# Kernel optimization log

Hardware: AMD Instinct MI355X
Metric: run time of the kernel (lower is better)

The kernel has to match this reference:

```python
import jax, jax.numpy as jnp
import numpy as np

B, T, H, V = 256, 256, 512, 32000
L = 3  # stacked LSTM layers


def setup_inputs() -> dict:
    key = jax.random.key(0)
    ks = jax.random.split(key, 12)
    s = 0.05
    n = lambda k, shp: (jax.random.normal(k, shp, jnp.float32) * s)
    return {
        "text_1": jax.random.randint(ks[0], (B, T), 0, V, dtype=jnp.int32),
        "text_2": jax.random.randint(ks[1], (B, T), 0, V, dtype=jnp.int32),
        "text_3": jax.random.randint(ks[2], (B, T), 0, V, dtype=jnp.int32),
        "emb": n(ks[3], (V, H)),
        "Wx": n(ks[4], (L, H, 4 * H)),
        "Wh": n(ks[5], (L, H, 4 * H)),
        "b": jnp.zeros((L, 4 * H), jnp.float32),
        "g1": jnp.ones((3 * H,), jnp.float32), "beta1": jnp.zeros((3 * H,), jnp.float32),
        "W1": n(ks[6], (3 * H, 2 * H)), "bd1": jnp.zeros((2 * H,), jnp.float32),
        "g2": jnp.ones((2 * H,), jnp.float32), "beta2": jnp.zeros((2 * H,), jnp.float32),
        "W2": n(ks[7], (2 * H, H // 5)), "bd2": jnp.zeros((H // 5,), jnp.float32),
        "g3": jnp.ones((H // 5,), jnp.float32), "beta3": jnp.zeros((H // 5,), jnp.float32),
        "W3": n(ks[8], (H // 5, 4)), "bd3": jnp.zeros((4,), jnp.float32),
    }


def _lstm_stack(tokens, emb, Wx, Wh, b):
    # tokens: [B, T] int -> last hidden of top layer [B, H]
    x = emb[tokens]                      # [B, T, H]
    x = jnp.transpose(x, (1, 0, 2))      # [T, B, H] (scan over time)
    bsz, h = x.shape[1], Wh.shape[1]
    for l in range(Wx.shape[0]):
        Wx_l, Wh_l, b_l = Wx[l], Wh[l], b[l]
        def step(carry, xt):
            hprev, cprev = carry
            gates = xt @ Wx_l + hprev @ Wh_l + b_l      # [B, 4H]
            i, f, g, o = jnp.split(gates, 4, axis=-1)
            c = jax.nn.sigmoid(f) * cprev + jax.nn.sigmoid(i) * jnp.tanh(g)
            hnew = jax.nn.sigmoid(o) * jnp.tanh(c)
            return (hnew, c), hnew
        init = (jnp.zeros((bsz, h), x.dtype), jnp.zeros((bsz, h), x.dtype))
        _, x = jax.lax.scan(step, init, x)
    return x[-1]                          # rnn_output[:, -1, :]


def _bn(x, gamma, beta, eps=1e-3):
    m = jnp.mean(x, axis=0)
    v = jnp.var(x, axis=0)
    return gamma * (x - m) * jax.lax.rsqrt(v + eps) + beta


def reference(text_1, text_2, text_3, emb, Wx, Wh, b,
              g1, beta1, W1, bd1, g2, beta2, W2, bd2, g3, beta3, W3, bd3):
    r1 = _lstm_stack(text_1, emb, Wx, Wh, b)
    r2 = _lstm_stack(text_2, emb, Wx, Wh, b)
    r3 = _lstm_stack(text_3, emb, Wx, Wh, b)
    r = jnp.concatenate([r1, r2, r3], axis=1)   # [B, 3H]
    r = _bn(r, g1, beta1)
    r = jax.nn.selu(r @ W1 + bd1)
    r = _bn(r, g2, beta2)
    r = jax.nn.selu(r @ W2 + bd2)
    r = _bn(r, g3, beta3)
    return r @ W3 + bd3                          # [B, 4] logits
```

## Files before the change

### kernel.cpp

```cpp
#include <hip/hip_runtime.h>
#include <hip/hip_bf16.h>

typedef __attribute__((ext_vector_type(8))) short short8;
typedef __attribute__((ext_vector_type(4))) float floatx4;

namespace {
constexpr int kB1 = 256;
constexpr int kT  = 256;
constexpr int kH  = 512;
constexpr int kL  = 3;
constexpr int kB3 = 768;
constexpr int kK  = 1024;
constexpr int kN  = 2048;
constexpr int kV  = 32000;
constexpr size_t kHB = (size_t)kB3 * kH;
constexpr int kRing = 16;
constexpr int kFenceP = 12;

constexpr size_t WREP_OFF   = 0;
constexpr size_t WREP_BYTES = (size_t)kL * kK * kN * 2;
constexpr size_t BREP_OFF   = WREP_OFF + WREP_BYTES;
constexpr size_t BREP_BYTES = (size_t)kL * kN * 4;
constexpr size_t EMB_OFF    = BREP_OFF + BREP_BYTES;
constexpr size_t EMB_BYTES  = (size_t)kV * kH * 2;
constexpr size_t HBUF_OFF   = EMB_OFF + EMB_BYTES;
constexpr size_t HBUF_BYTES = (size_t)kL * kRing * kHB * 2;
constexpr size_t CBUF_OFF   = HBUF_OFF + HBUF_BYTES;
constexpr size_t CBUF_BYTES = (size_t)kL * kHB * 4;
constexpr size_t BNA_OFF    = CBUF_OFF + CBUF_BYTES;
constexpr size_t BNC_OFF    = BNA_OFF + 1536 * 4;
constexpr size_t Z1_OFF     = BNC_OFF + 1536 * 4;
constexpr size_t Z2_OFF     = Z1_OFF + (size_t)256 * 1024 * 4;
constexpr size_t FLAG_OFF   = Z2_OFF + (size_t)256 * 102 * 4;
constexpr size_t BAR_OFF    = FLAG_OFF + 128;
constexpr size_t WS_NEEDED  = BAR_OFF + 4096;
constexpr int kPersistGrid  = 192;
}

__device__ __forceinline__ float ldf(const void* p, size_t idx, int isf32) {
  if (isf32) return ((const float*)p)[idx];
  return __bfloat162float(((const __hip_bfloat16*)p)[idx]);
}

__device__ __forceinline__ short f2bs(float x) {
  union { __hip_bfloat16 h; short s; } u;
  u.h = __float2bfloat16(x);
  return u.s;
}

__device__ __forceinline__ short8 cvt8(const float* q) {
  float4 lo = *(const float4*)q;
  float4 hi = *(const float4*)(q + 4);
  short8 v;
  v[0] = f2bs(lo.x); v[1] = f2bs(lo.y); v[2] = f2bs(lo.z); v[3] = f2bs(lo.w);
  v[4] = f2bs(hi.x); v[5] = f2bs(hi.y); v[6] = f2bs(hi.z); v[7] = f2bs(hi.w);
  return v;
}

__global__ void detect_kernel(const unsigned* __restrict__ g1, int* __restrict__ flag,
                              unsigned* __restrict__ bar) {
  int tid = threadIdx.x;
#pragma unroll
  for (int i = 0; i < 4; i++)
    __hip_atomic_store(&bar[tid + 256 * i], 0u, __ATOMIC_RELAXED, __HIP_MEMORY_SCOPE_AGENT);
  if (tid == 0 && blockIdx.x == 0)
    *flag = (g1[0] == 0x3F800000u) ? 1 : 0;
}

__global__ __launch_bounds__(256) void repack_kernel(
    const void* __restrict__ Wx, const void* __restrict__ Wh,
    const void* __restrict__ bias, const int* __restrict__ flagp,
    __hip_bfloat16* __restrict__ Wrep, float* __restrict__ brep) {
  int isf32 = *flagp;
  int idx = blockIdx.x * 256 + threadIdx.x;
  if (idx >= kL * kK * kN) return;
  int j  = idx & 7;
  int n2 = (idx >> 3) & (kN - 1);
  int kg = (idx >> 14) & 127;
  int l  = idx >> 21;
  int k  = kg * 8 + j;
  int ntile = n2 >> 7, c = n2 & 127, g = c >> 5, ul = c & 31;
  int u = ntile * 32 + ul;
  int col = g * 512 + u;
  float v;
  if (k < kH) v = ldf(Wx, ((size_t)l * kH + k) * kN + col, isf32);
  else        v = ldf(Wh, ((size_t)l * kH + (k - kH)) * kN + col, isf32);
  Wrep[idx] = __float2bfloat16(v);
  if (kg == 0 && j == 0) brep[l * kN + n2] = ldf(bias, (size_t)l * kN + col, isf32);
}

__global__ __launch_bounds__(256) void embrep_kernel(
    const void* __restrict__ emb, const int* __restrict__ flagp,
    __hip_bfloat16* __restrict__ er) {
  int isf32 = *flagp;
  size_t base = ((size_t)blockIdx.x * 256 + threadIdx.x) * 8;
  if (base >= (size_t)kV * kH) return;
  if (isf32) *(short8*)(er + base) = cvt8((const float*)emb + base);
  else       *(short8*)(er + base) = *(const short8*)((const __hip_bfloat16*)emb + base);
}

__device__ __forceinline__ void wait8(const unsigned* fp, unsigned target) {
  const int lane = threadIdx.x & 7;
  long long t0 = (long long)__builtin_amdgcn_s_memrealtime();
  int it = 0;
  for (;;) {
    unsigned v;
    asm volatile("global_load_dword %0, %1, off sc0 sc1\n\ts_waitcnt vmcnt(0)"
                 : "=v"(v) : "v"(fp + lane));
    if (__all(v >= target)) break;
    __builtin_amdgcn_s_sleep(1);
    if (((++it) & 31) == 0 &&
        (long long)__builtin_amdgcn_s_memrealtime() - t0 > 20000000LL) break;
  }
}

__global__ __launch_bounds__(1024) void persist_kernel(
    const __hip_bfloat16* __restrict__ Wrep, const float* __restrict__ brep,
    __hip_bfloat16* __restrict__ hbuf, const __hip_bfloat16* __restrict__ er,
    const int* __restrict__ flagp, const int* __restrict__ t1,
    const int* __restrict__ t2, const int* __restrict__ t3,
    unsigned* __restrict__ bar) {
  __shared__ __align__(16) char smem[24576 + 4 * 96 * 66 * 4];
  float* gl = (float*)(smem + 24576);

  const int tid = threadIdx.x;
  const int bid = blockIdx.x;
  const int xcd = bid & 7;
  const int j_  = bid >> 3;
  const int l   = j_ >> 3;
  const int r_  = j_ & 7;
  const int c_  = (xcd + 5 * l) & 7;
  const int mt  = (c_ >> 2) * 4 + (r_ & 3);
  const int nt  = (c_ & 3) * 2 + (r_ >> 4 ? 0 : (r_ >> 2));
  const int nt2 = (c_ & 3) * 2 + (r_ >> 2);
  const int ntF = nt2;

  unsigned* prod = bar;
  unsigned* myflag = prod + ((l * 8 + mt) * 8 + ntF);
  const unsigned* grpSelf  = prod + (l * 8 + mt) * 8;
  const unsigned* grpBelow = (l > 0) ? prod + ((l - 1) * 8 + mt) * 8 : nullptr;
  const unsigned* grpAbove = (l < 2) ? prod + ((l + 1) * 8 + mt) * 8 : nullptr;

  const int wv = tid >> 6, lane = tid & 63, lm = lane & 15, lq = lane >> 4;
  const int mrow = (wv >> 3) * 48;
  const int ncol = ntF * 256 + (wv & 7) * 32;

  const int r0 = tid >> 3;
  const int c8 = tid & 7;
  const bool stg = (tid < 768);
  const int R  = mt * 96 + r0;
  const unsigned ro = (unsigned)R * kH + c8 * 8;

  const int* tb = nullptr;
  int tk = 0;
  if (l == 0 && stg) {
    tb = (((R >> 8) == 0) ? t1 : ((R >> 8) == 1) ? t2 : t3) + (R & 255) * kT;
    tk = tb[0];
  }

  const __hip_bfloat16* WB = Wrep + (size_t)l * kK * kN;
  const float bv0 = brep[l * kN + ncol + lm];
  const float bv1 = brep[l * kN + ncol + 16 + lm];

  char* aw = smem + r0 * 128 + ((c8 ^ (r0 & 7)) << 4);
  int oswz[2];
#pragma unroll
  for (int kk = 0; kk < 2; kk++) oswz[kk] = (((kk * 4 + lq) ^ (lm & 7)) << 4);

  const int cuu = tid & 63, crb = tid >> 6;
  float creg[6] = {0.f, 0.f, 0.f, 0.f, 0.f, 0.f};

  short8 aCur, aNxt;
  short8 bA[2][2], bB[2][2];
  const __hip_bfloat16* xe = nullptr;
  if (l == 0 && stg) xe = er + (size_t)tk * kH + c8 * 8;

#pragma unroll 1
  for (int s = 0; s < kT + kL - 1; s++) {
    const int t = s - l;
    if (t >= kT) break;
    if (t >= 0) {
      const __hip_bfloat16* hp = hbuf + ((size_t)l * kRing + ((t + kRing - 1) & (kRing - 1))) * kHB;
      const __hip_bfloat16* xh = nullptr;
      int nk = 0;
      if (l == 0) {
        if (stg && t + 1 < kT) nk = tb[t + 1];
      } else {
        xh = hbuf + ((size_t)(l - 1) * kRing + (t & (kRing - 1))) * kHB;
      }

      auto loadA = [&](int p, short8& d) {
        if (!stg) return;
        if (p < 8) {
          if (l == 0) d = *(const short8*)(xe + p * 64);
          else        d = *(const short8*)(xh + ro + p * 64);
        } else if (t == 0) {
          short8 z = {0, 0, 0, 0, 0, 0, 0, 0};
          d = z;
        } else {
          d = *(const short8*)(hp + ro + (p - 8) * 64);
        }
      };
      auto loadB = [&](int p, short8 (&bf)[2][2]) {
#pragma unroll
        for (int kk = 0; kk < 2; kk++)
#pragma unroll
          for (int nf = 0; nf < 2; nf++) {
            int kg = p * 8 + kk * 4 + lq;
            bf[kk][nf] = *(const short8*)(WB + ((size_t)kg * kN + ncol + nf * 16 + lm) * 8);
          }
      };

      if (l > 0) wait8(grpBelow, (unsigned)(t + 1));
      if (l != 0 || t == 0) loadA(0, aCur);
      if (t == 0) loadB(0, bA);

      floatx4 zf = {0.f, 0.f, 0.f, 0.f};
      floatx4 acc[3][2];
#pragma unroll
      for (int a = 0; a < 3; a++) { acc[a][0] = zf; acc[a][1] = zf; }

#pragma unroll
      for (int si = 0; si < 16; si++) {
        const int buf = si & 1;
        if (stg) *(short8*)(aw + buf * 12288) = aCur;
        __syncthreads();
        if (si < 15) {
          if (si == 7 && t > 0) wait8(grpSelf, (unsigned)t);
          loadA(si + 1, aNxt);
          if (buf == 0) loadB(si + 1, bB); else loadB(si + 1, bA);
        }
        const char* arb = smem + buf * 12288 + lm * 128;
#pragma unroll
        for (int kk = 0; kk < 2; kk++) {
          const short8* bf = buf ? &bB[kk][0] : &bA[kk][0];
          short8 af0 = *(const short8*)(arb + (mrow + 0) * 128 + oswz[kk]);
          short8 af1 = *(const short8*)(arb + (mrow + 16) * 128 + oswz[kk]);
          short8 af2 = *(const short8*)(arb + (mrow + 32) * 128 + oswz[kk]);
          acc[0][0] = __builtin_amdgcn_mfma_f32_16x16x32_bf16(af0, bf[0], acc[0][0], 0, 0, 0);
          acc[0][1] = __builtin_amdgcn_mfma_f32_16x16x32_bf16(af0, bf[1], acc[0][1], 0, 0, 0);
          acc[1][0] = __builtin_amdgcn_mfma_f32_16x16x32_bf16(af1, bf[0], acc[1][0], 0, 0, 0);
          acc[1][1] = __builtin_amdgcn_mfma_f32_16x16x32_bf16(af1, bf[1], acc[1][1], 0, 0, 0);
          acc[2][0] = __builtin_amdgcn_mfma_f32_16x16x32_bf16(af2, bf[0], acc[2][0], 0, 0, 0);
          acc[2][1] = __builtin_amdgcn_mfma_f32_16x16x32_bf16(af2, bf[1], acc[2][1], 0, 0, 0);
        }
        aCur = aNxt;
      }

#pragma unroll
      for (int mf = 0; mf < 3; mf++)
#pragma unroll
        for (int nf = 0; nf < 2; nf++)
#pragma unroll
          for (int r = 0; r < 4; r++) {
            int rowf = mrow + mf * 16 + lq * 4 + r;
            int ct = (wv & 7) * 32 + nf * 16 + lm;
            int ut = ct >> 7, cc = ct & 127;
            int g = cc >> 5, ul = ut * 32 + (cc & 31);
            gl[((size_t)g * 96 + rowf) * 66 + ul] = acc[mf][nf][r] + (nf ? bv1 : bv0);
          }
      __syncthreads();

      if (l < 2 && t >= kRing) wait8(grpAbove, (unsigned)(t - (kRing - 1)));

      __hip_bfloat16* hout = hbuf + ((size_t)l * kRing + (t & (kRing - 1))) * kHB;
#pragma unroll
      for (int ii = 0; ii < 6; ii++) {
        int rowf = crb + 16 * ii;
        float gi = fminf(fmaxf(gl[(0 * 96 + rowf) * 66 + cuu], -40.f), 40.f);
        float gf = fminf(fmaxf(gl[(1 * 96 + rowf) * 66 + cuu], -40.f), 40.f);
        float gg = fminf(fmaxf(gl[(2 * 96 + rowf) * 66 + cuu], -40.f), 40.f);
        float go = fminf(fmaxf(gl[(3 * 96 + rowf) * 66 + cuu], -40.f), 40.f);
        float c_old = (t > 0) ? creg[ii] : 0.f;
        float si = 1.f / (1.f + __expf(-gi));
        float sf = 1.f / (1.f + __expf(-gf));
        float so = 1.f / (1.f + __expf(-go));
        float cn = sf * c_old + si * tanhf(gg);
        float hn = so * tanhf(cn);
        creg[ii] = cn;
        union { __hip_bfloat16 h; unsigned short u; } cv;
        cv.h = __float2bfloat16(hn);
        __hip_atomic_store(
            (unsigned short*)(hout + (size_t)(mt * 96 + rowf) * kH + ntF * 64 + cuu),
            cv.u, __ATOMIC_RELAXED, __HIP_MEMORY_SCOPE_AGENT);
      }

      __syncthreads();
      if (tid == 0)
        __hip_atomic_store(myflag, (unsigned)(t + 1), __ATOMIC_RELEASE,
                           __HIP_MEMORY_SCOPE_AGENT);

      if (t + 1 < kT) {
        loadB(0, bA);
        if (l == 0 && stg) {
          tk = nk;
          xe = er + (size_t)tk * kH + c8 * 8;
          loadA(0, aCur);
        }
      }
    }
    if (s < kT + kL - 2 && (s % kFenceP) == (kFenceP - 1))
      __builtin_amdgcn_fence(__ATOMIC_ACQUIRE, "agent");
  }
  (void)nt;
}

__global__ __launch_bounds__(256) void step_kernel(
    int s,
    const __hip_bfloat16* __restrict__ Wrep, const float* __restrict__ brep,
    __hip_bfloat16* __restrict__ hbuf, float* __restrict__ cbuf,
    const void* __restrict__ emb, const int* __restrict__ flagp,
    const int* __restrict__ t1, const int* __restrict__ t2, const int* __restrict__ t3) {
  __shared__ __align__(16) char smem[34816];

  int bid = blockIdx.x;
  int l  = bid / 192;
  int rr = bid % 192;
  int nt = rr & 15;
  int mt = rr >> 4;
  int t = s - l;
  if (t < 0 || t >= kT) return;

  int isf32 = *flagp;
  int tid = threadIdx.x;
  int wv = tid >> 6, lane = tid & 63;
  int lm = lane & 15, lq = lane >> 4;

  int arow = tid >> 2;
  int kc   = tid & 3;
  int row_g = mt * 64 + arow;

  const void* xsrc;
  bool xf32 = false;
  if (l == 0) {
    int i = row_g >> 8, bb = row_g & 255;
    const int* txt = (i == 0) ? t1 : (i == 1) ? t2 : t3;
    int tok = txt[bb * kT + t];
    if (isf32) { xsrc = (const void*)((const float*)emb + (size_t)tok * kH); xf32 = true; }
    else         xsrc = (const void*)((const __hip_bfloat16*)emb + (size_t)tok * kH);
  } else {
    const __hip_bfloat16* hIn = hbuf + ((size_t)(l - 1) * kRing + (t & (kRing - 1))) * kHB;
    xsrc = (const void*)(hIn + (size_t)row_g * kH);
  }
  const __hip_bfloat16* hrow = nullptr;
  if (t > 0) {
    const __hip_bfloat16* hPrev = hbuf + ((size_t)l * kRing + ((t + kRing - 1) & (kRing - 1))) * kHB;
    hrow = hPrev + (size_t)row_g * kH;
  }

  floatx4 zf = {0.f, 0.f, 0.f, 0.f};
  floatx4 acc[4][2];
#pragma unroll
  for (int a = 0; a < 4; a++)
#pragma unroll
    for (int b = 0; b < 2; b++) acc[a][b] = zf;

  const __hip_bfloat16* WB = Wrep + (size_t)l * kK * kN;
  int n0w = nt * 128 + wv * 32;

#pragma unroll 1
  for (int sl = 0; sl < 8; sl++) {
    short8 bfrag[4][2];
#pragma unroll
    for (int kk = 0; kk < 4; kk++)
#pragma unroll
      for (int nf = 0; nf < 2; nf++) {
        size_t kg = (size_t)(sl * 16 + kk * 4 + lq);
        const __hip_bfloat16* p = WB + (kg * kN + (n0w + nf * 16 + lm)) * 8;
        bfrag[kk][nf] = *(const short8*)p;
      }
    short8 av[4];
    bool zero = (sl >= 4) && (t == 0);
    if (!zero) {
      if (sl < 4 && xf32) {
        const float* sf = (const float*)xsrc + sl * 128;
#pragma unroll
        for (int jj = 0; jj < 4; jj++) {
          const float* q = sf + kc * 8 + jj * 32;
          float4 lo = *(const float4*)q;
          float4 hi = *(const float4*)(q + 4);
          short8 v;
          v[0] = f2bs(lo.x); v[1] = f2bs(lo.y); v[2] = f2bs(lo.z); v[3] = f2bs(lo.w);
          v[4] = f2bs(hi.x); v[5] = f2bs(hi.y); v[6] = f2bs(hi.z); v[7] = f2bs(hi.w);
          av[jj] = v;
        }
      } else {
        const __hip_bfloat16* src = (sl < 4)
            ? ((const __hip_bfloat16*)xsrc + sl * 128)
            : (hrow + (sl - 4) * 128);
#pragma unroll
        for (int jj = 0; jj < 4; jj++)
          av[jj] = *(const short8*)(src + kc * 8 + jj * 32);
      }
    } else {
      short8 vz = {0, 0, 0, 0, 0, 0, 0, 0};
#pragma unroll
      for (int jj = 0; jj < 4; jj++) av[jj] = vz;
    }
    __syncthreads();
#pragma unroll
    for (int jj = 0; jj < 4; jj++) {
      int klocal = kc * 8 + jj * 32;
      *(short8*)(smem + arow * 272 + klocal * 2) = av[jj];
    }
    __syncthreads();
#pragma unroll
    for (int kk = 0; kk < 4; kk++) {
      short8 afrag[4];
#pragma unroll
      for (int mf = 0; mf < 4; mf++) {
        int rowf = mf * 16 + lm;
        afrag[mf] = *(const short8*)(smem + rowf * 272 + kk * 64 + lq * 16);
      }
#pragma unroll
      for (int mf = 0; mf < 4; mf++)
#pragma unroll
        for (int nf = 0; nf < 2; nf++)
          acc[mf][nf] = __builtin_amdgcn_mfma_f32_16x16x32_bf16(
              afrag[mf], bfrag[kk][nf], acc[mf][nf], 0, 0, 0);
    }
  }

  const float* bl = brep + l * kN;
#pragma unroll
  for (int nf = 0; nf < 2; nf++) {
    float bv = bl[n0w + nf * 16 + lm];
#pragma unroll
    for (int mf = 0; mf < 4; mf++)
#pragma unroll
      for (int r = 0; r < 4; r++) acc[mf][nf][r] += bv;
  }

  __syncthreads();
  float* gl = (float*)smem;
#pragma unroll
  for (int mf = 0; mf < 4; mf++)
#pragma unroll
    for (int nf = 0; nf < 2; nf++)
#pragma unroll
      for (int r = 0; r < 4; r++) {
        int rowf = mf * 16 + lq * 4 + r;
        int uu   = nf * 16 + lm;
        gl[((size_t)wv * 64 + rowf) * 34 + uu] = acc[mf][nf][r];
      }
  __syncthreads();

  float* cl = cbuf + (size_t)l * kHB;
  __hip_bfloat16* hout = hbuf + ((size_t)l * kRing + (t & (kRing - 1))) * kHB;
#pragma unroll
  for (int ii = 0; ii < 8; ii++) {
    int idx = tid + 256 * ii;
    int uu = idx & 31, rowf = idx >> 5;
    float gi = fminf(fmaxf(gl[(0 * 64 + rowf) * 34 + uu], -40.f), 40.f);
    float gf = fminf(fmaxf(gl[(1 * 64 + rowf) * 34 + uu], -40.f), 40.f);
    float gg = fminf(fmaxf(gl[(2 * 64 + rowf) * 34 + uu], -40.f), 40.f);
    float go = fminf(fmaxf(gl[(3 * 64 + rowf) * 34 + uu], -40.f), 40.f);
    int bg = mt * 64 + rowf;
    int ug = nt * 32 + uu;
    size_t off = (size_t)bg * kH + ug;
    float c_old = (t > 0) ? cl[off] : 0.f;
    float si = 1.f / (1.f + __expf(-gi));
    float sf = 1.f / (1.f + __expf(-gf));
    float so = 1.f / (1.f + __expf(-go));
    float cn = sf * c_old + si * tanhf(gg);
    float hn = so * tanhf(cn);
    cl[off] = cn;
    hout[off] = __float2bfloat16(hn);
  }
}

__global__ __launch_bounds__(256) void stats_kernel(
    int ncols, int mode, const void* __restrict__ src,
    const void* __restrict__ gamma, const void* __restrict__ beta,
    const int* __restrict__ flagp, float* __restrict__ bn_a, float* __restrict__ bn_c) {
  int isf32 = *flagp;
  int col = blockIdx.x * 256 + threadIdx.x;
  if (col >= ncols) return;
  float sum = 0.f, ss = 0.f;
  for (int b = 0; b < kB1; b++) {
    float v;
    if (mode == 0) {
      const __hip_bfloat16* h = (const __hip_bfloat16*)src;
      v = __bfloat162float(h[((size_t)((col >> 9) * kB1 + b)) * kH + (col & 511)]);
    } else {
      v = ((const float*)src)[(size_t)b * ncols + col];
    }
    v = fmaxf(-1e15f, fminf(v, 1e15f));
    sum += v; ss += v * v;
  }
  float mean = sum * (1.f / kB1);
  float var  = ss * (1.f / kB1) - mean * mean;
  float a = ldf(gamma, col, isf32) * rsqrtf(var + 1e-3f);
  bn_a[col] = a;
  bn_c[col] = ldf(beta, col, isf32) - mean * a;
}

__global__ __launch_bounds__(256) void headgemm_kernel(
    int Kd, int Nd, int mode, const void* __restrict__ Asrc,
    const float* __restrict__ bn_a, const float* __restrict__ bn_c,
    const void* __restrict__ W, const void* __restrict__ bias,
    const int* __restrict__ flagp, float* __restrict__ out, int do_selu) {
  __shared__ float As[32][65];
  __shared__ float Bs[32][65];
  int isf32 = *flagp;
  int tid = threadIdx.x;
  int bx = blockIdx.x, by = blockIdx.y;
  int tx = tid & 15, ty = tid >> 4;
  float acc[4][4] = {};
  int am = tid & 63, ak = tid >> 6;
  int bk = tid >> 3, bn8 = (tid & 7) * 8;
  for (int ks = 0; ks < Kd; ks += 32) {
    __syncthreads();
    for (int jj = 0; jj < 8; jj++) {
      int kl = ak * 8 + jj;
      int kg = ks + kl;
      int mg = by * 64 + am;
      float v;
      if (mode == 0) {
        const __hip_bfloat16* h = (const __hip_bfloat16*)Asrc;
        v = __bfloat162float(h[((size_t)((kg >> 9) * kB1 + mg)) * kH + (kg & 511)]);
      } else {
        v = ((const float*)Asrc)[(size_t)mg * Kd + kg];
      }
      As[kl][am] = v * bn_a[kg] + bn_c[kg];
    }
    for (int e = 0; e < 8; e++) {
      int col = bx * 64 + bn8 + e;
      Bs[bk][bn8 + e] = (col < Nd) ? ldf(W, (size_t)(ks + bk) * Nd + col, isf32) : 0.f;
    }
    __syncthreads();
    for (int k = 0; k < 32; k++) {
      float ar[4], br[4];
#pragma unroll
      for (int i = 0; i < 4; i++) ar[i] = As[k][ty * 4 + i];
#pragma unroll
      for (int j = 0; j < 4; j++) br[j] = Bs[k][tx * 4 + j];
#pragma unroll
      for (int i = 0; i < 4; i++)
#pragma unroll
        for (int j = 0; j < 4; j++) acc[i][j] += ar[i] * br[j];
    }
  }
  for (int i = 0; i < 4; i++) {
    int row = by * 64 + ty * 4 + i;
    for (int j = 0; j < 4; j++) {
      int col = bx * 64 + tx * 4 + j;
      if (col < Nd) {
        float y = acc[i][j] + ldf(bias, col, isf32);
        if (do_selu)
          y = (y > 0.f) ? 1.0507009873554805f * y
                        : 1.0507009873554805f * 1.6732632423543772f * (__expf(y) - 1.f);
        out[(size_t)row * Nd + col] = y;
      }
    }
  }
}

__global__ __launch_bounds__(256) void final_kernel(
    const float* __restrict__ z2, const float* __restrict__ bn_a, const float* __restrict__ bn_c,
    const void* __restrict__ W3, const void* __restrict__ bd3,
    const int* __restrict__ flagp, void* __restrict__ out) {
  int isf32 = *flagp;
  int b = threadIdx.x;
  float acc[4] = {0.f, 0.f, 0.f, 0.f};
  for (int j = 0; j < 102; j++) {
    float y = z2[b * 102 + j] * bn_a[j] + bn_c[j];
#pragma unroll
    for (int g = 0; g < 4; g++) acc[g] += y * ldf(W3, j * 4 + g, isf32);
  }
#pragma unroll
  for (int g = 0; g < 4; g++) {
    float y = acc[g] + ldf(bd3, g, isf32);
    if (isf32) ((float*)out)[b * 4 + g] = y;
    else ((__hip_bfloat16*)out)[b * 4 + g] = __float2bfloat16(y);
  }
}

extern "C" void kernel_launch(void* const* d_in, const int* in_sizes, int n_in,
                              void* d_out, int out_size, void* d_ws, size_t ws_size,
                              hipStream_t stream) {
  const int* t1 = (const int*)d_in[0];
  const int* t2 = (const int*)d_in[1];
  const int* t3 = (const int*)d_in[2];
  const void* emb = d_in[3];
  const void* Wx  = d_in[4];
  const void* Wh  = d_in[5];
  const void* bb  = d_in[6];
  const void* g1  = d_in[7];
  const void* be1 = d_in[8];
  const void* W1  = d_in[9];
  const void* bd1 = d_in[10];
  const void* g2  = d_in[11];
  const void* be2 = d_in[12];
  const void* W2  = d_in[13];
  const void* bd2 = d_in[14];
  const void* g3  = d_in[15];
  const void* be3 = d_in[16];
  const void* W3  = d_in[17];
  const void* bd3 = d_in[18];

  char* ws = (char*)d_ws;
  __hip_bfloat16* Wrep = (__hip_bfloat16*)(ws + WREP_OFF);
  float* brep = (float*)(ws + BREP_OFF);
  __hip_bfloat16* embrep = (__hip_bfloat16*)(ws + EMB_OFF);
  __hip_bfloat16* hbuf = (__hip_bfloat16*)(ws + HBUF_OFF);
  float* cbuf = (float*)(ws + CBUF_OFF);
  float* bn_a = (float*)(ws + BNA_OFF);
  float* bn_c = (float*)(ws + BNC_OFF);
  float* z1 = (float*)(ws + Z1_OFF);
  float* z2 = (float*)(ws + Z2_OFF);
  int* flag = (int*)(ws + FLAG_OFF);
  unsigned* bar = (unsigned*)(ws + BAR_OFF);

  static int persist_ok = -1;
  if (persist_ok < 0) {
    int nb = 0, ncu = 0, dev = 0;
    (void)hipGetDevice(&dev);
    (void)hipDeviceGetAttribute(&ncu, hipDeviceAttributeMultiprocessorCount, dev);
    hipError_t e = hipOccupancyMaxActiveBlocksPerMultiprocessor(&nb, persist_kernel, 1024, 0);
    persist_ok = (e == hipSuccess && (long)nb * (long)ncu >= kPersistGrid &&
                  ws_size >= WS_NEEDED) ? 1 : 0;
  }

  detect_kernel<<<1, 256, 0, stream>>>((const unsigned*)g1, flag, bar);

  repack_kernel<<<(kL * kK * kN) / 256, 256, 0, stream>>>(Wx, Wh, bb, flag, Wrep, brep);
  embrep_kernel<<<(kV * kH) / (256 * 8), 256, 0, stream>>>(emb, flag, embrep);

  if (persist_ok) {
    persist_kernel<<<kPersistGrid, 1024, 0, stream>>>(
        Wrep, brep, hbuf, embrep, flag, t1, t2, t3, bar);
  } else {
    for (int s = 0; s < kT + kL - 1; s++)
      step_kernel<<<3 * 192, 256, 0, stream>>>(s, Wrep, brep, hbuf, cbuf, emb, flag, t1, t2, t3);
  }

  const __hip_bfloat16* hTop = hbuf + (size_t)(2 * kRing + ((kT - 1) & (kRing - 1))) * kHB;
  stats_kernel<<<6, 256, 0, stream>>>(1536, 0, hTop, g1, be1, flag, bn_a, bn_c);
  headgemm_kernel<<<dim3(16, 4), 256, 0, stream>>>(1536, 1024, 0, hTop, bn_a, bn_c, W1, bd1, flag, z1, 1);
  stats_kernel<<<4, 256, 0, stream>>>(1024, 1, z1, g2, be2, flag, bn_a, bn_c);
  headgemm_kernel<<<dim3(2, 4), 256, 0, stream>>>(1024, 102, 1, z1, bn_a, bn_c, W2, bd2, flag, z2, 1);
  stats_kernel<<<1, 256, 0, stream>>>(102, 1, z2, g3, be3, flag, bn_a, bn_c);
  final_kernel<<<1, 256, 0, stream>>>(z2, bn_a, bn_c, W3, bd3, flag, (void*)d_out);
}
```

Before: 6.012 ms.

## Deepen A-operand prefetch to four slices and centralize dependency waits in one wave

Each timestep now does both the below-layer and self-layer dependency waits up front in wave 0, followed by a block barrier, instead of having every thread spin and placing the self wait mid-loop. The A operand is prefetched four slices ahead in a register ring rather than one. The cross-step prefetch of the next token embedding and the first weight slice is removed, so those loads are now issued at the start of each step. The aim is to cut redundant polling and hide global load latency better, at the cost of no longer overlapping x-input loads with the hidden-state dependency wait and of extra registers.

```diff
diff --git a/kernel.cpp b/kernel.cpp
--- a/kernel.cpp
+++ b/kernel.cpp
@@ -131,9 +131,7 @@
   const int r_  = j_ & 7;
   const int c_  = (xcd + 5 * l) & 7;
   const int mt  = (c_ >> 2) * 4 + (r_ & 3);
-  const int nt  = (c_ & 3) * 2 + (r_ >> 4 ? 0 : (r_ >> 2));
-  const int nt2 = (c_ & 3) * 2 + (r_ >> 2);
-  const int ntF = nt2;
+  const int ntF = (c_ & 3) * 2 + (r_ >> 2);
 
   unsigned* prod = bar;
   unsigned* myflag = prod + ((l * 8 + mt) * 8 + ntF);
@@ -152,11 +150,8 @@
   const unsigned ro = (unsigned)R * kH + c8 * 8;
 
   const int* tb = nullptr;
-  int tk = 0;
-  if (l == 0 && stg) {
+  if (l == 0 && stg)
     tb = (((R >> 8) == 0) ? t1 : ((R >> 8) == 1) ? t2 : t3) + (R & 255) * kT;
-    tk = tb[0];
-  }
 
   const __hip_bfloat16* WB = Wrep + (size_t)l * kK * kN;
   const float bv0 = brep[l * kN + ncol + lm];
@@ -170,10 +165,7 @@
   const int cuu = tid & 63, crb = tid >> 6;
   float creg[6] = {0.f, 0.f, 0.f, 0.f, 0.f, 0.f};
 
-  short8 aCur, aNxt;
   short8 bA[2][2], bB[2][2];
-  const __hip_bfloat16* xe = nullptr;
-  if (l == 0 && stg) xe = er + (size_t)tk * kH + c8 * 8;
 
 #pragma unroll 1
   for (int s = 0; s < kT + kL - 1; s++) {
@@ -181,15 +173,18 @@
     if (t >= kT) break;
     if (t >= 0) {
       const __hip_bfloat16* hp = hbuf + ((size_t)l * kRing + ((t + kRing - 1) & (kRing - 1))) * kHB;
-      const __hip_bfloat16* xh = nullptr;
-      int nk = 0;
-      if (l == 0) {
-        if (stg && t + 1 < kT) nk = tb[t + 1];
-      } else {
-        xh = hbuf + ((size_t)(l - 1) * kRing + (t & (kRing - 1))) * kHB;
-      }
-
-      auto loadA = [&](int p, short8& d) {
+      const __hip_bfloat16* xh = (l > 0)
+          ? hbuf + ((size_t)(l - 1) * kRing + (t & (kRing - 1))) * kHB : nullptr;
+      const __hip_bfloat16* xe = nullptr;
+      if (l == 0 && stg) xe = er + (size_t)tb[t] * kH + c8 * 8;
+
+      if (wv == 0) {
+        if (l > 0) wait8(grpBelow, (unsigned)(t + 1));
+        if (t > 0) wait8(grpSelf, (unsigned)t);
+      }
+      __syncthreads();
+
+      auto loadSlice = [&](int p, short8& d) {
         if (!stg) return;
         if (p < 8) {
           if (l == 0) d = *(const short8*)(xe + p * 64);
@@ -211,9 +206,10 @@
           }
       };
 
-      if (l > 0) wait8(grpBelow, (unsigned)(t + 1));
-      if (l != 0 || t == 0) loadA(0, aCur);
-      if (t == 0) loadB(0, bA);
+      short8 aP[4];
+#pragma unroll
+      for (int p = 0; p < 4; p++) loadSlice(p, aP[p]);
+      loadB(0, bA);
 
       floatx4 zf = {0.f, 0.f, 0.f, 0.f};
       floatx4 acc[3][2];
@@ -223,11 +219,11 @@
 #pragma unroll
       for (int si = 0; si < 16; si++) {
         const int buf = si & 1;
-        if (stg) *(short8*)(aw + buf * 12288) = aCur;
+        const int slot = si & 3;
+        if (stg) *(short8*)(aw + buf * 12288) = aP[slot];
         __syncthreads();
+        if (si < 12) loadSlice(si + 4, aP[slot]);
         if (si < 15) {
-          if (si == 7 && t > 0) wait8(grpSelf, (unsigned)t);
-          loadA(si + 1, aNxt);
           if (buf == 0) loadB(si + 1, bB); else loadB(si + 1, bA);
         }
         const char* arb = smem + buf * 12288 + lm * 128;
@@ -244,7 +240,6 @@
           acc[2][0] = __builtin_amdgcn_mfma_f32_16x16x32_bf16(af2, bf[0], acc[2][0], 0, 0, 0);
           acc[2][1] = __builtin_amdgcn_mfma_f32_16x16x32_bf16(af2, bf[1], acc[2][1], 0, 0, 0);
         }
-        aCur = aNxt;
       }
 
 #pragma unroll
@@ -261,7 +256,10 @@
           }
       __syncthreads();
 
-      if (l < 2 && t >= kRing) wait8(grpAbove, (unsigned)(t - (kRing - 1)));
+      if (l < 2 && t >= kRing) {
+        if (wv == 0) wait8(grpAbove, (unsigned)(t - (kRing - 1)));
+        __syncthreads();
+      }
 
       __hip_bfloat16* hout = hbuf + ((size_t)l * kRing + (t & (kRing - 1))) * kHB;
 #pragma unroll
@@ -289,20 +287,10 @@
       if (tid == 0)
         __hip_atomic_store(myflag, (unsigned)(t + 1), __ATOMIC_RELEASE,
                            __HIP_MEMORY_SCOPE_AGENT);
-
-      if (t + 1 < kT) {
-        loadB(0, bA);
-        if (l == 0 && stg) {
-          tk = nk;
-          xe = er + (size_t)tk * kH + c8 * 8;
-          loadA(0, aCur);
-        }
-      }
     }
     if (s < kT + kL - 2 && (s % kFenceP) == (kFenceP - 1))
       __builtin_amdgcn_fence(__ATOMIC_ACQUIRE, "agent");
   }
-  (void)nt;
 }
 
 __global__ __launch_bounds__(256) void step_kernel(
```

Measured after the change: 6.178 ms. 1.03x slower.
